# Kernel optimization log

Measured on AMD Instinct MI355X. Metric: run time of the kernel, lower is better.

Reference implementation:

```python
import jax, jax.numpy as jnp
import numpy as np

H = 16
D_MODEL = 1024
D_K = D_MODEL // H
B, S = 4, 2048


def setup_inputs() -> dict:
    key = jax.random.key(0)
    ks = jax.random.split(key, 12)
    scale = 1.0 / np.sqrt(D_MODEL)
    inp = {
        "q": jax.random.normal(ks[0], (B, S, D_MODEL), dtype=jnp.float32),
        "k": jax.random.normal(ks[1], (B, S, D_MODEL), dtype=jnp.float32),
        "v": jax.random.normal(ks[2], (B, S, D_MODEL), dtype=jnp.float32),
        # torch nn.Linear weights: shape (out, in), y = x @ W.T + b
        "Wq": jax.random.uniform(ks[3], (D_MODEL, D_MODEL), minval=-scale, maxval=scale),
        "bq": jax.random.uniform(ks[4], (D_MODEL,), minval=-scale, maxval=scale),
        "Wk": jax.random.uniform(ks[5], (D_MODEL, D_MODEL), minval=-scale, maxval=scale),
        "bk": jax.random.uniform(ks[6], (D_MODEL,), minval=-scale, maxval=scale),
        "Wv": jax.random.uniform(ks[7], (D_MODEL, D_MODEL), minval=-scale, maxval=scale),
        "bv": jax.random.uniform(ks[8], (D_MODEL,), minval=-scale, maxval=scale),
        "Wo": jax.random.uniform(ks[9], (D_MODEL, D_MODEL), minval=-scale, maxval=scale),
        "bo": jax.random.uniform(ks[10], (D_MODEL,), minval=-scale, maxval=scale),
        "ln_g": jnp.ones((D_MODEL,), dtype=jnp.float32),
        "ln_b": jnp.zeros((D_MODEL,), dtype=jnp.float32),
    }
    return inp


def _layernorm(x, g, b, eps=1e-5):
    mu = jnp.mean(x, axis=-1, keepdims=True)
    var = jnp.var(x, axis=-1, keepdims=True)
    return (x - mu) * jax.lax.rsqrt(var + eps) * g + b


def reference(q, k, v, Wq, bq, Wk, bk, Wv, bv, Wo, bo, ln_g, ln_b):
    nb = q.shape[0]
    # projections, split heads -> (B, H, S, d_k)
    def proj(x, W, b):
        y = x @ W.T + b
        return y.reshape(nb, -1, H, D_K).transpose(0, 2, 1, 3)

    Q = proj(q, Wq, bq)
    K = proj(k, Wk, bk)
    V = proj(v, Wv, bv)

    scores = jnp.einsum("bhqd,bhkd->bhqk", Q, K) / jnp.sqrt(jnp.float32(D_K))
    p_attn = jax.nn.softmax(scores, axis=-1)
    x = jnp.einsum("bhqk,bhkd->bhqd", p_attn, V)
    x = x.transpose(0, 2, 1, 3).reshape(nb, -1, H * D_K)
    out = _layernorm(x @ Wo.T + bo + q, ln_g, ln_b)
    return out
```

## Files before the change

kernel.cpp:

```cpp
#include <hip/hip_runtime.h>

#define DM 1024
#define NH 16
#define DK 64
#define SEQ 2048
#define BATCH 4
#define M_TOT (BATCH * SEQ)

typedef short s16x8 __attribute__((ext_vector_type(8)));
typedef float f32x4 __attribute__((ext_vector_type(4)));
typedef unsigned int u32x4 __attribute__((ext_vector_type(4)));
typedef unsigned int u32x2 __attribute__((ext_vector_type(2)));

#define MFMA16(a, b, c) __builtin_amdgcn_mfma_f32_16x16x32_bf16((a), (b), (c), 0, 0, 0)

#define QSCALE 0.1803368801111244f

__device__ __forceinline__ float bf2f(unsigned short u) {
    return __uint_as_float(((unsigned int)u) << 16);
}
__device__ __forceinline__ unsigned short f2bf(float f) {
    unsigned int u = __float_as_uint(f);
    u += 0x7FFFu + ((u >> 16) & 1u);
    return (unsigned short)(u >> 16);
}
__device__ __forceinline__ unsigned int pack_bf2(unsigned int lo, unsigned int hi) {
    return ((lo + 0x8000u) >> 16) | ((hi + 0x8000u) & 0xFFFF0000u);
}
__device__ __forceinline__ unsigned int pack_bf2_trunc(float lo, float hi) {
    return __builtin_amdgcn_perm(__float_as_uint(hi), __float_as_uint(lo), 0x07060302u);
}
__device__ __forceinline__ s16x8 load_cvt8(const float* p) {
    u32x4 x0 = *reinterpret_cast<const u32x4*>(p);
    u32x4 x1 = *reinterpret_cast<const u32x4*>(p + 4);
    union { s16x8 v; unsigned int u[4]; } r;
    r.u[0] = pack_bf2(x0[0], x0[1]);
    r.u[1] = pack_bf2(x0[2], x0[3]);
    r.u[2] = pack_bf2(x1[0], x1[1]);
    r.u[3] = pack_bf2(x1[2], x1[3]);
    return r.v;
}

__device__ __forceinline__ void ld_lds16(const unsigned short* g, unsigned short* lds_base) {
    __builtin_amdgcn_global_load_lds(
        (const __attribute__((address_space(1))) unsigned int*)g,
        (__attribute__((address_space(3))) unsigned int*)lds_base,
        16, 0, 0);
}

__global__ __launch_bounds__(256) void cvt_bf16_kernel(
    const float* __restrict__ src, unsigned short* __restrict__ dst, int n)
{
    const int i = (blockIdx.x * 256 + threadIdx.x) * 8;
    if (i >= n) return;
    *reinterpret_cast<s16x8*>(dst + i) = load_cvt8(src + i);
}

__global__ __launch_bounds__(256) void cvt_w_kernel(
    const float* __restrict__ w0, const float* __restrict__ w1,
    const float* __restrict__ w2, const float* __restrict__ w3,
    unsigned short* __restrict__ dst)
{
    const float* src = blockIdx.y == 0 ? w0 : blockIdx.y == 1 ? w1
                     : blockIdx.y == 2 ? w2 : w3;
    const long off = (long)blockIdx.y * ((long)DM * DM);
    const int i = (blockIdx.x * 256 + threadIdx.x) * 8;
    *reinterpret_cast<s16x8*>(dst + off + i) = load_cvt8(src + i);
}

__global__ __launch_bounds__(256) void gemm_kernel(
    const unsigned short* __restrict__ Ab,
    const unsigned short* __restrict__ Wb,
    const float* __restrict__ bias,
    unsigned short* __restrict__ Y,
    const int mode, const float scale)
{
    const int tid  = threadIdx.x;
    const int lane = tid & 63;
    const int wave = tid >> 6;
    const int c16  = lane & 15;
    const int quad = lane >> 4;
    const int m0 = blockIdx.x * 128;
    const int n0 = blockIdx.y * 128;
    const int wm = (wave >> 1) * 64;
    const int wn = (wave & 1) * 64;

    __shared__ __align__(16) unsigned short As[128 * 32];
    __shared__ __align__(16) unsigned short Bs[128 * 32];

    f32x4 acc[4][4];
    #pragma unroll
    for (int tm = 0; tm < 4; ++tm)
        #pragma unroll
        for (int tn = 0; tn < 4; ++tn) acc[tm][tn] = (f32x4){0.f, 0.f, 0.f, 0.f};

    int srow[2], sch[2];
    #pragma unroll
    for (int c = 0; c < 2; ++c) {
        const int s = c * 256 + wave * 64 + lane;
        srow[c] = s >> 2;
        sch[c]  = s & 3;
    }

    for (int k0 = 0; k0 < DM; k0 += 32) {
        #pragma unroll
        for (int c = 0; c < 2; ++c) {
            unsigned short* abase = As + (c * 256 + wave * 64) * 8;
            unsigned short* bbase = Bs + (c * 256 + wave * 64) * 8;
            ld_lds16(Ab + (long)(m0 + srow[c]) * DM + k0 + sch[c] * 8, abase);
            ld_lds16(Wb + (long)(n0 + srow[c]) * DM + k0 + sch[c] * 8, bbase);
        }
        __syncthreads();

        s16x8 a[4], b[4];
        #pragma unroll
        for (int tm = 0; tm < 4; ++tm)
            a[tm] = *reinterpret_cast<const s16x8*>(As + (wm + tm * 16 + c16) * 32 + quad * 8);
        #pragma unroll
        for (int tn = 0; tn < 4; ++tn)
            b[tn] = *reinterpret_cast<const s16x8*>(Bs + (wn + tn * 16 + c16) * 32 + quad * 8);
        #pragma unroll
        for (int tm = 0; tm < 4; ++tm)
            #pragma unroll
            for (int tn = 0; tn < 4; ++tn)
                acc[tm][tn] = MFMA16(a[tm], b[tn], acc[tm][tn]);
        __syncthreads();
    }

    #pragma unroll
    for (int tn = 0; tn < 4; ++tn) {
        const int col = n0 + wn + tn * 16 + c16;
        const float bv = bias[col];
        const int h = col >> 6, d = col & 63;
        #pragma unroll
        for (int tm = 0; tm < 4; ++tm) {
            #pragma unroll
            for (int r = 0; r < 4; ++r) {
                const int m = m0 + wm + tm * 16 + quad * 4 + r;
                const int b_ = m >> 11;
                const int s  = m & 2047;
                const float v = (acc[tm][tn][r] + bv) * scale;
                long idx;
                if (mode == 0)      idx = (((long)(b_ * NH + h) * SEQ + s) * DK) + d;
                else if (mode == 1) idx = (((long)(b_ * NH + h) * DK + d) * SEQ) + s;
                else                idx = (long)m * DM + col;
                Y[idx] = f2bf(v);
            }
        }
    }
}

__global__ __launch_bounds__(256, 4) void attn_kernel(
    const unsigned short* __restrict__ Qh,
    const unsigned short* __restrict__ Kh,
    const unsigned short* __restrict__ Vt,
    unsigned short* __restrict__ Xo)
{
    const int lane = threadIdx.x & 63;
    const int wave = threadIdx.x >> 6;
    const int c16  = lane & 15;
    const int quad = lane >> 4;
    const int bh = blockIdx.x;
    const int b_ = bh >> 4, h = bh & 15;
    const int m0 = blockIdx.y * 128 + wave * 32;

    __shared__ __align__(16) unsigned short Ks[2 * 64 * 64];
    __shared__ __align__(16) unsigned short Vs[2 * 64 * 64];

    const unsigned short* Kbh = Kh + (long)bh * SEQ * DK;
    const unsigned short* Vbh = Vt + (long)bh * DK * SEQ;

    s16x8 bQ[2][2];
    #pragma unroll
    for (int qt = 0; qt < 2; ++qt) {
        const unsigned short* qb = Qh + ((long)bh * SEQ + m0 + qt * 16 + c16) * DK + quad * 8;
        bQ[qt][0] = *reinterpret_cast<const s16x8*>(qb);
        bQ[qt][1] = *reinterpret_cast<const s16x8*>(qb + 32);
    }

    f32x4 o[2][4];
    #pragma unroll
    for (int qt = 0; qt < 2; ++qt)
        #pragma unroll
        for (int c = 0; c < 4; ++c) o[qt][c] = (f32x4){0.f, 0.f, 0.f, 0.f};
    float li[2] = {0.f, 0.f};

    int st_n[4], st_x[4], st_isK[4];
    #pragma unroll
    for (int j = 0; j < 4; ++j) {
        const int c = wave * 4 + j;
        const int s = (c & 7) * 64 + lane;
        st_isK[j] = (c < 8);
        st_n[j] = s >> 3;
        st_x[j] = (s & 7) ^ (st_n[j] & 7);
    }

    auto stage = [&](int buf, int n0) {
        #pragma unroll
        for (int j = 0; j < 4; ++j) {
            const int c = wave * 4 + j;
            if (st_isK[j])
                ld_lds16(Kbh + (n0 + st_n[j]) * DK + st_x[j] * 8,
                         &Ks[buf * 4096 + (c & 7) * 512]);
            else
                ld_lds16(Vbh + (long)st_n[j] * SEQ + n0 + st_x[j] * 8,
                         &Vs[buf * 4096 + (c & 7) * 512]);
        }
    };

    stage(0, 0);
    __syncthreads();

    for (int it = 0; it < SEQ / 64; ++it) {
        const int cur = it & 1;
        if (it + 1 < SEQ / 64) stage(cur ^ 1, (it + 1) * 64);

        const unsigned short* Kb = Ks + cur * 4096;
        const unsigned short* Vb = Vs + cur * 4096;

        f32x4 st[2][4];
        #pragma unroll
        for (int t = 0; t < 4; ++t) {
            const int n = t * 16 + c16;
            const int sw = n & 7;
            s16x8 a0 = *reinterpret_cast<const s16x8*>(&Kb[n * 64 + ((quad ^ sw) * 8)]);
            s16x8 a1 = *reinterpret_cast<const s16x8*>(&Kb[n * 64 + (((quad + 4) ^ sw) * 8)]);
            #pragma unroll
            for (int qt = 0; qt < 2; ++qt) {
                f32x4 s = (f32x4){0.f, 0.f, 0.f, 0.f};
                s = MFMA16(a0, bQ[qt][0], s);
                s = MFMA16(a1, bQ[qt][1], s);
                st[qt][t] = s;
            }
        }

        s16x8 bP[2][2];
        #pragma unroll
        for (int qt = 0; qt < 2; ++qt) {
            float psum = 0.f;
            #pragma unroll
            for (int t = 0; t < 4; ++t)
                #pragma unroll
                for (int r = 0; r < 4; ++r) {
                    const float p = exp2f(st[qt][t][r]);
                    st[qt][t][r] = p;
                    psum += p;
                }
            li[qt] += psum;

            uint2 w[4];
            #pragma unroll
            for (int t = 0; t < 4; ++t) {
                w[t].x = pack_bf2_trunc(st[qt][t][0], st[qt][t][1]);
                w[t].y = pack_bf2_trunc(st[qt][t][2], st[qt][t][3]);
            }
            #pragma unroll
            for (int hh = 0; hh < 2; ++hh) {
                u32x2 s0 = __builtin_amdgcn_permlane32_swap(w[2 * hh].x, w[2 * hh + 1].x, false, false);
                u32x2 s1 = __builtin_amdgcn_permlane32_swap(w[2 * hh].y, w[2 * hh + 1].y, false, false);
                u32x2 t0 = __builtin_amdgcn_permlane16_swap(s0[0], s0[1], false, false);
                u32x2 t1 = __builtin_amdgcn_permlane16_swap(s1[0], s1[1], false, false);
                union { s16x8 v; unsigned int u[4]; } f;
                f.u[0] = t0[0];
                f.u[1] = t1[0];
                f.u[2] = t0[1];
                f.u[3] = t1[1];
                bP[qt][hh] = f.v;
            }
        }

        #pragma unroll
        for (int cc = 0; cc < 4; ++cc) {
            const int d = cc * 16 + c16;
            const int sw = d & 7;
            s16x8 a0 = *reinterpret_cast<const s16x8*>(&Vb[d * 64 + ((quad ^ sw) * 8)]);
            s16x8 a1 = *reinterpret_cast<const s16x8*>(&Vb[d * 64 + (((quad + 4) ^ sw) * 8)]);
            #pragma unroll
            for (int qt = 0; qt < 2; ++qt) {
                o[qt][cc] = MFMA16(a0, bP[qt][0], o[qt][cc]);
                o[qt][cc] = MFMA16(a1, bP[qt][1], o[qt][cc]);
            }
        }
        __syncthreads();
    }

    #pragma unroll
    for (int qt = 0; qt < 2; ++qt) {
        float l = li[qt];
        l += __shfl_xor(l, 16, 64);
        l += __shfl_xor(l, 32, 64);
        const float inv = 1.f / l;
        unsigned short* orow = Xo + ((long)b_ * SEQ + m0 + qt * 16 + c16) * DM + h * DK;
        #pragma unroll
        for (int c = 0; c < 4; ++c) {
            uint2 w;
            w.x = pack_bf2(__float_as_uint(o[qt][c][0] * inv), __float_as_uint(o[qt][c][1] * inv));
            w.y = pack_bf2(__float_as_uint(o[qt][c][2] * inv), __float_as_uint(o[qt][c][3] * inv));
            *reinterpret_cast<uint2*>(orow + c * 16 + quad * 4) = w;
        }
    }
}

__global__ __launch_bounds__(256) void ln_kernel(
    const unsigned short* __restrict__ Xlin,
    const float* __restrict__ qres,
    const float* __restrict__ g,
    const float* __restrict__ bb,
    float* __restrict__ out)
{
    const int row = blockIdx.x;
    const int tid = threadIdx.x;
    const int c0 = tid * 4;
    const int lane = tid & 63, wave = tid >> 6;

    __shared__ float ssum[4], ssq[4];

    uint2 xb = *reinterpret_cast<const uint2*>(Xlin + (long)row * DM + c0);
    float4 qv = *reinterpret_cast<const float4*>(qres + (long)row * DM + c0);
    float v[4];
    v[0] = bf2f((unsigned short)(xb.x & 0xFFFF)) + qv.x;
    v[1] = bf2f((unsigned short)(xb.x >> 16))    + qv.y;
    v[2] = bf2f((unsigned short)(xb.y & 0xFFFF)) + qv.z;
    v[3] = bf2f((unsigned short)(xb.y >> 16))    + qv.w;

    float s = v[0] + v[1] + v[2] + v[3];
    float q2 = v[0]*v[0] + v[1]*v[1] + v[2]*v[2] + v[3]*v[3];
    #pragma unroll
    for (int d = 1; d < 64; d <<= 1) {
        s  += __shfl_xor(s, d, 64);
        q2 += __shfl_xor(q2, d, 64);
    }
    if (lane == 0) { ssum[wave] = s; ssq[wave] = q2; }
    __syncthreads();
    const float ts = ssum[0] + ssum[1] + ssum[2] + ssum[3];
    const float tq = ssq[0] + ssq[1] + ssq[2] + ssq[3];
    const float mu = ts * (1.f / 1024.f);
    const float var = tq * (1.f / 1024.f) - mu * mu;
    const float rstd = rsqrtf(var + 1e-5f);

    float4 gv = *reinterpret_cast<const float4*>(g + c0);
    float4 bv = *reinterpret_cast<const float4*>(bb + c0);
    float4 o;
    o.x = (v[0] - mu) * rstd * gv.x + bv.x;
    o.y = (v[1] - mu) * rstd * gv.y + bv.y;
    o.z = (v[2] - mu) * rstd * gv.z + bv.z;
    o.w = (v[3] - mu) * rstd * gv.w + bv.w;
    *reinterpret_cast<float4*>(out + (long)row * DM + c0) = o;
}

extern "C" void kernel_launch(void* const* d_in, const int* in_sizes, int n_in,
                              void* d_out, int out_size, void* d_ws, size_t ws_size,
                              hipStream_t stream) {
    const float* q   = (const float*)d_in[0];
    const float* k   = (const float*)d_in[1];
    const float* v   = (const float*)d_in[2];
    const float* Wq  = (const float*)d_in[3];
    const float* bq  = (const float*)d_in[4];
    const float* Wk  = (const float*)d_in[5];
    const float* bk  = (const float*)d_in[6];
    const float* Wv  = (const float*)d_in[7];
    const float* bvv = (const float*)d_in[8];
    const float* Wo  = (const float*)d_in[9];
    const float* bo  = (const float*)d_in[10];
    const float* lng = (const float*)d_in[11];
    const float* lnb = (const float*)d_in[12];

    unsigned short* ws = (unsigned short*)d_ws;
    const long WE = (long)DM * DM;
    const long NE = (long)M_TOT * DM;
    unsigned short* Wqb = ws;
    unsigned short* Wkb = Wqb + WE;
    unsigned short* Wvb = Wkb + WE;
    unsigned short* Wob = Wvb + WE;
    unsigned short* U1  = Wob + WE;
    unsigned short* U2  = U1 + NE;
    unsigned short* U3  = U2 + NE;
    unsigned short* U4  = U3 + NE;

    dim3 blk(256);
    const int cvtW = (int)(WE / 2048);
    const int cvtX = (int)(NE / 2048);
    cvt_w_kernel<<<dim3(cvtW, 4), blk, 0, stream>>>(Wq, Wk, Wv, Wo, Wqb);

    dim3 ggemm(M_TOT / 128, DM / 128);
    cvt_bf16_kernel<<<cvtX, blk, 0, stream>>>(q, U1, (int)NE);
    gemm_kernel<<<ggemm, blk, 0, stream>>>(U1, Wqb, bq, U2, 0, QSCALE);
    cvt_bf16_kernel<<<cvtX, blk, 0, stream>>>(k, U1, (int)NE);
    gemm_kernel<<<ggemm, blk, 0, stream>>>(U1, Wkb, bk, U3, 0, 1.0f);
    cvt_bf16_kernel<<<cvtX, blk, 0, stream>>>(v, U1, (int)NE);
    gemm_kernel<<<ggemm, blk, 0, stream>>>(U1, Wvb, bvv, U4, 1, 1.0f);

    attn_kernel<<<dim3(BATCH * NH, SEQ / 128), blk, 0, stream>>>(U2, U3, U4, U1);

    gemm_kernel<<<ggemm, blk, 0, stream>>>(U1, Wob, bo, U2, 2, 1.0f);
    ln_kernel<<<dim3(M_TOT), blk, 0, stream>>>(U2, q, lng, lnb, (float*)d_out);
}
```

Before: 417.3 us.

## Batch QKV conversion and GEMMs, compute softmax row sums via MFMA, add setprio

When the workspace is large enough, the three input conversions and the three projection GEMMs are merged into single launches over a z-dimension. This cuts launch count and fills the GPU with one 3x larger grid. In attention, the per-row softmax denominator is now accumulated with an MFMA against a ones matrix, replacing scalar adds and the final shuffles, and s_setprio raises wave priority around the MFMA sections. The fallback path keeps the old sequence if the workspace is too small, and the MFMA row sum sums the bf16-truncated probabilities instead of the fp32 values.

```diff
diff --git a/kernel.cpp b/kernel.cpp
--- a/kernel.cpp
+++ b/kernel.cpp
@@ -56,6 +56,16 @@
     *reinterpret_cast<s16x8*>(dst + i) = load_cvt8(src + i);
 }
 
+__global__ __launch_bounds__(256) void cvt3_kernel(
+    const float* __restrict__ s0, const float* __restrict__ s1,
+    const float* __restrict__ s2, unsigned short* __restrict__ dst)
+{
+    const float* src = blockIdx.z == 0 ? s0 : blockIdx.z == 1 ? s1 : s2;
+    const long off = (long)blockIdx.z * ((long)M_TOT * DM);
+    const int i = (blockIdx.x * 256 + threadIdx.x) * 8;
+    *reinterpret_cast<s16x8*>(dst + off + i) = load_cvt8(src + i);
+}
+
 __global__ __launch_bounds__(256) void cvt_w_kernel(
     const float* __restrict__ w0, const float* __restrict__ w1,
     const float* __restrict__ w2, const float* __restrict__ w3,
@@ -68,7 +78,7 @@
     *reinterpret_cast<s16x8*>(dst + off + i) = load_cvt8(src + i);
 }
 
-__global__ __launch_bounds__(256) void gemm_kernel(
+__device__ __forceinline__ void gemm_body(
     const unsigned short* __restrict__ Ab,
     const unsigned short* __restrict__ Wb,
     const float* __restrict__ bias,
@@ -150,6 +160,35 @@
     }
 }
 
+__global__ __launch_bounds__(256) void gemm_kernel(
+    const unsigned short* __restrict__ Ab,
+    const unsigned short* __restrict__ Wb,
+    const float* __restrict__ bias,
+    unsigned short* __restrict__ Y,
+    const int mode, const float scale)
+{
+    gemm_body(Ab, Wb, bias, Y, mode, scale);
+}
+
+__global__ __launch_bounds__(256) void gemm3_kernel(
+    const unsigned short* __restrict__ A3,
+    const unsigned short* __restrict__ W3,
+    const float* __restrict__ bq, const float* __restrict__ bk,
+    const float* __restrict__ bv,
+    unsigned short* __restrict__ Y3)
+{
+    const int z = blockIdx.z;
+    const long NE = (long)M_TOT * DM;
+    const long WEl = (long)DM * DM;
+    const unsigned short* Ab = A3 + (long)z * NE;
+    const unsigned short* Wb = W3 + (long)z * WEl;
+    const float* bias = z == 0 ? bq : z == 1 ? bk : bv;
+    unsigned short* Y = Y3 + (long)z * NE;
+    const int mode = (z == 2) ? 1 : 0;
+    const float scale = (z == 0) ? QSCALE : 1.0f;
+    gemm_body(Ab, Wb, bias, Y, mode, scale);
+}
+
 __global__ __launch_bounds__(256, 4) void attn_kernel(
     const unsigned short* __restrict__ Qh,
     const unsigned short* __restrict__ Kh,
@@ -178,12 +217,19 @@
         bQ[qt][1] = *reinterpret_cast<const s16x8*>(qb + 32);
     }
 
+    union { s16x8 v; unsigned int u[4]; } onesu;
+    onesu.u[0] = 0x3F803F80u; onesu.u[1] = 0x3F803F80u;
+    onesu.u[2] = 0x3F803F80u; onesu.u[3] = 0x3F803F80u;
+    const s16x8 onesA = onesu.v;
+
     f32x4 o[2][4];
-    #pragma unroll
-    for (int qt = 0; qt < 2; ++qt)
+    f32x4 lacc[2];
+    #pragma unroll
+    for (int qt = 0; qt < 2; ++qt) {
         #pragma unroll
         for (int c = 0; c < 4; ++c) o[qt][c] = (f32x4){0.f, 0.f, 0.f, 0.f};
-    float li[2] = {0.f, 0.f};
+        lacc[qt] = (f32x4){0.f, 0.f, 0.f, 0.f};
+    }
 
     int st_n[4], st_x[4], st_isK[4];
     #pragma unroll
@@ -219,6 +265,7 @@
         const unsigned short* Vb = Vs + cur * 4096;
 
         f32x4 st[2][4];
+        __builtin_amdgcn_s_setprio(1);
         #pragma unroll
         for (int t = 0; t < 4; ++t) {
             const int n = t * 16 + c16;
@@ -233,20 +280,16 @@
                 st[qt][t] = s;
             }
         }
+        __builtin_amdgcn_s_setprio(0);
 
         s16x8 bP[2][2];
         #pragma unroll
         for (int qt = 0; qt < 2; ++qt) {
-            float psum = 0.f;
             #pragma unroll
             for (int t = 0; t < 4; ++t)
                 #pragma unroll
-                for (int r = 0; r < 4; ++r) {
-                    const float p = exp2f(st[qt][t][r]);
-                    st[qt][t][r] = p;
-                    psum += p;
-                }
-            li[qt] += psum;
+                for (int r = 0; r < 4; ++r)
+                    st[qt][t][r] = exp2f(st[qt][t][r]);
 
             uint2 w[4];
             #pragma unroll
@@ -269,6 +312,12 @@
             }
         }
 
+        __builtin_amdgcn_s_setprio(1);
+        #pragma unroll
+        for (int qt = 0; qt < 2; ++qt) {
+            lacc[qt] = MFMA16(onesA, bP[qt][0], lacc[qt]);
+            lacc[qt] = MFMA16(onesA, bP[qt][1], lacc[qt]);
+        }
         #pragma unroll
         for (int cc = 0; cc < 4; ++cc) {
             const int d = cc * 16 + c16;
@@ -281,15 +330,13 @@
                 o[qt][cc] = MFMA16(a1, bP[qt][1], o[qt][cc]);
             }
         }
+        __builtin_amdgcn_s_setprio(0);
         __syncthreads();
     }
 
     #pragma unroll
     for (int qt = 0; qt < 2; ++qt) {
-        float l = li[qt];
-        l += __shfl_xor(l, 16, 64);
-        l += __shfl_xor(l, 32, 64);
-        const float inv = 1.f / l;
+        const float inv = 1.f / lacc[qt][0];
         unsigned short* orow = Xo + ((long)b_ * SEQ + m0 + qt * 16 + c16) * DM + h * DK;
         #pragma unroll
         for (int c = 0; c < 4; ++c) {
@@ -368,30 +415,49 @@
     unsigned short* ws = (unsigned short*)d_ws;
     const long WE = (long)DM * DM;
     const long NE = (long)M_TOT * DM;
-    unsigned short* Wqb = ws;
-    unsigned short* Wkb = Wqb + WE;
-    unsigned short* Wvb = Wkb + WE;
-    unsigned short* Wob = Wvb + WE;
-    unsigned short* U1  = Wob + WE;
-    unsigned short* U2  = U1 + NE;
-    unsigned short* U3  = U2 + NE;
-    unsigned short* U4  = U3 + NE;
 
     dim3 blk(256);
     const int cvtW = (int)(WE / 2048);
     const int cvtX = (int)(NE / 2048);
-    cvt_w_kernel<<<dim3(cvtW, 4), blk, 0, stream>>>(Wq, Wk, Wv, Wo, Wqb);
-
     dim3 ggemm(M_TOT / 128, DM / 128);
-    cvt_bf16_kernel<<<cvtX, blk, 0, stream>>>(q, U1, (int)NE);
-    gemm_kernel<<<ggemm, blk, 0, stream>>>(U1, Wqb, bq, U2, 0, QSCALE);
-    cvt_bf16_kernel<<<cvtX, blk, 0, stream>>>(k, U1, (int)NE);
-    gemm_kernel<<<ggemm, blk, 0, stream>>>(U1, Wkb, bk, U3, 0, 1.0f);
-    cvt_bf16_kernel<<<cvtX, blk, 0, stream>>>(v, U1, (int)NE);
-    gemm_kernel<<<ggemm, blk, 0, stream>>>(U1, Wvb, bvv, U4, 1, 1.0f);
-
-    attn_kernel<<<dim3(BATCH * NH, SEQ / 128), blk, 0, stream>>>(U2, U3, U4, U1);
-
-    gemm_kernel<<<ggemm, blk, 0, stream>>>(U1, Wob, bo, U2, 2, 1.0f);
-    ln_kernel<<<dim3(M_TOT), blk, 0, stream>>>(U2, q, lng, lnb, (float*)d_out);
-}
+
+    const size_t need_batched = (size_t)(4 * WE + 6 * NE) * sizeof(unsigned short);
+
+    if (ws_size >= need_batched) {
+        unsigned short* Wqb = ws;
+        unsigned short* Wob = Wqb + 3 * WE;
+        unsigned short* A3  = Wqb + 4 * WE;
+        unsigned short* O3  = A3 + 3 * NE;
+        unsigned short* Xo   = A3;
+        unsigned short* Xlin = A3 + NE;
+
+        cvt_w_kernel<<<dim3(cvtW, 4), blk, 0, stream>>>(Wq, Wk, Wv, Wo, Wqb);
+        cvt3_kernel<<<dim3(cvtX, 1, 3), blk, 0, stream>>>(q, k, v, A3);
+        gemm3_kernel<<<dim3(M_TOT / 128, DM / 128, 3), blk, 0, stream>>>(
+            A3, Wqb, bq, bk, bvv, O3);
+        attn_kernel<<<dim3(BATCH * NH, SEQ / 128), blk, 0, stream>>>(
+            O3, O3 + NE, O3 + 2 * NE, Xo);
+        gemm_kernel<<<ggemm, blk, 0, stream>>>(Xo, Wob, bo, Xlin, 2, 1.0f);
+        ln_kernel<<<dim3(M_TOT), blk, 0, stream>>>(Xlin, q, lng, lnb, (float*)d_out);
+    } else {
+        unsigned short* Wqb = ws;
+        unsigned short* Wkb = Wqb + WE;
+        unsigned short* Wvb = Wkb + WE;
+        unsigned short* Wob = Wvb + WE;
+        unsigned short* U1  = Wob + WE;
+        unsigned short* U2  = U1 + NE;
+        unsigned short* U3  = U2 + NE;
+        unsigned short* U4  = U3 + NE;
+
+        cvt_w_kernel<<<dim3(cvtW, 4), blk, 0, stream>>>(Wq, Wk, Wv, Wo, Wqb);
+        cvt_bf16_kernel<<<cvtX, blk, 0, stream>>>(q, U1, (int)NE);
+        gemm_kernel<<<ggemm, blk, 0, stream>>>(U1, Wqb, bq, U2, 0, QSCALE);
+        cvt_bf16_kernel<<<cvtX, blk, 0, stream>>>(k, U1, (int)NE);
+        gemm_kernel<<<ggemm, blk, 0, stream>>>(U1, Wkb, bk, U3, 0, 1.0f);
+        cvt_bf16_kernel<<<cvtX, blk, 0, stream>>>(v, U1, (int)NE);
+        gemm_kernel<<<ggemm, blk, 0, stream>>>(U1, Wvb, bvv, U4, 1, 1.0f);
+        attn_kernel<<<dim3(BATCH * NH, SEQ / 128), blk, 0, stream>>>(U2, U3, U4, U1);
+        gemm_kernel<<<ggemm, blk, 0, stream>>>(U1, Wob, bo, U2, 2, 1.0f);
+        ln_kernel<<<dim3(M_TOT), blk, 0, stream>>>(U2, q, lng, lnb, (float*)d_out);
+    }
+}
```

After: 397.0 us. 1.05x faster.
